# Performance work log

Hardware: AMD Instinct MI355X
Metric: run time of the kernel (lower is better)

Reference implementation:

```python
import jax, jax.numpy as jnp
import numpy as np

B, S, EMB, H = 4, 1024, 1024, 16
HD = EMB // H          # head_dim = 64
MAXP = 512             # RelativePositionalEncoder default max_position


def setup_inputs() -> dict:
    key = jax.random.key(0)
    ks = jax.random.split(key, 13)
    s = 1.0 / np.sqrt(EMB)  # xavier-ish scale keeps softmax logits sane
    return {
        "query": jax.random.normal(ks[0], (B, S, EMB), jnp.float32),
        "key": jax.random.normal(ks[1], (B, S, EMB), jnp.float32),
        "value": jax.random.normal(ks[2], (B, S, EMB), jnp.float32),
        "Wq": jax.random.normal(ks[3], (EMB, EMB), jnp.float32) * s,
        "bq": jnp.zeros((EMB,), jnp.float32),
        "Wk": jax.random.normal(ks[4], (EMB, EMB), jnp.float32) * s,
        "bk": jnp.zeros((EMB,), jnp.float32),
        "Wv": jax.random.normal(ks[5], (EMB, EMB), jnp.float32) * s,
        "bv": jnp.zeros((EMB,), jnp.float32),
        "Wo": jax.random.normal(ks[6], (EMB, EMB), jnp.float32) * s,
        "bo": jnp.zeros((EMB,), jnp.float32),
        "rel_k": jax.random.normal(ks[7], (2 * MAXP + 1, HD), jnp.float32) * 0.05,
        "rel_v": jax.random.normal(ks[8], (2 * MAXP + 1, HD), jnp.float32) * 0.05,
    }


def _split_heads(x):
    # [B,S,E] -> [B,S,H,HD] -> [B,H,S,HD] -> [B*H,S,HD]
    return x.reshape(B, S, H, HD).transpose(0, 2, 1, 3).reshape(B * H, S, HD)


def reference(query, key, value, Wq, bq, Wk, bk, Wv, bv, Wo, bo, rel_k, rel_v):
    scale = jnp.sqrt(jnp.asarray(HD, query.dtype))
    q = _split_heads(query @ Wq + bq)
    k = _split_heads(key @ Wk + bk)
    v = _split_heads(value @ Wv + bv)
    # relative position lookup tables: [Sq, Sk, HD]
    rp = jnp.clip(jnp.arange(S)[None, :] - jnp.arange(S)[:, None], -MAXP, MAXP) + MAXP
    a_key = rel_k[rp]
    a_value = rel_v[rp]
    qk = jnp.einsum('bqd,bkd->bqk', q, k)              # [B*H,S,S]
    rel_qk = jnp.einsum('bqd,qkd->bqk', q, a_key)      # relative score term
    attn = jax.nn.softmax((qk + rel_qk) / scale, axis=-1)
    out = jnp.einsum('bqk,bkd->bqd', attn, v) + jnp.einsum('bqk,qkd->bqd', attn, a_value)
    # faithful to original's view(num_heads, batch, -1, head_dim) then concat reshape
    out = out.reshape(H, B, S, HD).transpose(0, 2, 1, 3).reshape(B, S, H * HD)
    out = out @ Wo + bo
    return (out, attn)
```

## Files before the change

kernel.cpp:

```cpp
#include <hip/hip_runtime.h>


using s16x8 = __attribute__((ext_vector_type(8))) short;
using f32x4 = __attribute__((ext_vector_type(4))) float;

#define MFMA16 __builtin_amdgcn_mfma_f32_16x16x32_bf16

__device__ __forceinline__ float bf2f(unsigned short u) {
  union { unsigned int u; float f; } v; v.u = ((unsigned int)u) << 16; return v.f;
}
__device__ __forceinline__ unsigned short f2bf(float f) {
  union { float f; unsigned int u; } v; v.f = f;
  unsigned int r = (v.u + 0x7FFFu + ((v.u >> 16) & 1u)) >> 16;
  return (unsigned short)r;
}

__global__ void k_cvt_bf16(const float* __restrict__ in, unsigned short* __restrict__ out, int n) {
  int i = (blockIdx.x * 256 + threadIdx.x) * 8;
  if (i >= n) return;
  float4 a = *(const float4*)(in + i);
  float4 b = *(const float4*)(in + i + 4);
  s16x8 o;
  o[0] = (short)f2bf(a.x); o[1] = (short)f2bf(a.y); o[2] = (short)f2bf(a.z); o[3] = (short)f2bf(a.w);
  o[4] = (short)f2bf(b.x); o[5] = (short)f2bf(b.y); o[6] = (short)f2bf(b.z); o[7] = (short)f2bf(b.w);
  *(s16x8*)(out + i) = o;
}

__global__ void k_tr1024(const float* __restrict__ W, unsigned short* __restrict__ Wt) {
  __shared__ float t[32][33];
  int tx = threadIdx.x, ty = threadIdx.y;
  int n0 = blockIdx.x * 32, k0 = blockIdx.y * 32;
#pragma unroll
  for (int r = 0; r < 4; ++r)
    t[ty * 4 + r][tx] = W[(size_t)(k0 + ty * 4 + r) * 1024 + n0 + tx];
  __syncthreads();
#pragma unroll
  for (int r = 0; r < 4; ++r)
    Wt[(size_t)(n0 + ty * 4 + r) * 1024 + k0 + tx] = f2bf(t[tx][ty * 4 + r]);
}

__global__ void k_relprep(const float* __restrict__ rk, const float* __restrict__ rv,
                          unsigned short* __restrict__ relkb, unsigned short* __restrict__ rvTb) {
  int b = blockIdx.x;
  if (b < 33) {
    int i = (b * 256 + threadIdx.x) * 8;
    if (i < 65600) {
      float4 a = *(const float4*)(rk + i);
      float4 c = *(const float4*)(rk + i + 4);
      s16x8 o;
      o[0] = (short)f2bf(a.x); o[1] = (short)f2bf(a.y); o[2] = (short)f2bf(a.z); o[3] = (short)f2bf(a.w);
      o[4] = (short)f2bf(c.x); o[5] = (short)f2bf(c.y); o[6] = (short)f2bf(c.z); o[7] = (short)f2bf(c.w);
      *(s16x8*)(relkb + i) = o;
    }
  } else {
    int i = (b - 33) * 256 + threadIdx.x;
    if (i < 65600) {
      int p = i >> 6, d = i & 63;
      rvTb[d * 1040 + p] = f2bf(rv[i]);
    }
  }
}

__global__ __launch_bounds__(256)
void k_trV(const unsigned short* __restrict__ v, unsigned short* __restrict__ vt) {
  __shared__ unsigned short T[64][72];
  const int tid = threadIdx.x;
  const int bh = blockIdx.x >> 4;
  const int s0 = (blockIdx.x & 15) << 6;
  const int r = tid >> 2, cb = (tid & 3) << 4;
  const unsigned short* src = v + ((size_t)bh << 16) + (size_t)(s0 + r) * 64 + cb;
  *(s16x8*)&T[r][cb] = *(const s16x8*)src;
  *(s16x8*)&T[r][cb + 8] = *(const s16x8*)(src + 8);
  __syncthreads();
  unsigned short* dst = vt + ((size_t)bh << 16) + (size_t)r * 1024 + s0 + cb;
  s16x8 o0, o1;
#pragma unroll
  for (int e = 0; e < 8; ++e) o0[e] = T[cb + e][r];
#pragma unroll
  for (int e = 0; e < 8; ++e) o1[e] = T[cb + 8 + e][r];
  *(s16x8*)dst = o0;
  *(s16x8*)(dst + 8) = o1;
}

template <int MODE>
__global__ __launch_bounds__(256, 2)
void k_gemm(const unsigned short* __restrict__ A, const unsigned short* __restrict__ BT,
            const float* __restrict__ bias, void* __restrict__ Cout) {
  __shared__ alignas(16) unsigned short aT[2][4096];
  __shared__ alignas(16) unsigned short bT[2][2048];
  const int tid = threadIdx.x;
  const int lane = tid & 63;
  const int l15 = lane & 15, lhi = lane >> 4;
  const int w = tid >> 6;
  const int wr = w * 32;
  const int brow = blockIdx.y * 128, bcol = blockIdx.x * 64;
  f32x4 acc[2][4] = {};

#define STAGE(buf, kt) do {                                                              \
    int k0s = (kt) * 32;                                                                 \
    {                                                                                    \
      int c = tid;                                                                       \
      int row = c >> 2, k8 = (c & 3) * 8;                                                \
      __builtin_amdgcn_global_load_lds(                                                  \
        (const __attribute__((address_space(1))) void*)(A + (size_t)(brow + row) * 1024 + k0s + k8), \
        (__attribute__((address_space(3))) void*)(&aT[buf][c * 8]), 16, 0, 0);           \
      __builtin_amdgcn_global_load_lds(                                                  \
        (const __attribute__((address_space(1))) void*)(BT + (size_t)(bcol + row) * 1024 + k0s + k8),\
        (__attribute__((address_space(3))) void*)(&bT[buf][c * 8]), 16, 0, 0);           \
    }                                                                                    \
    {                                                                                    \
      int c = tid + 256;                                                                 \
      int row = c >> 2, k8 = (c & 3) * 8;                                                \
      __builtin_amdgcn_global_load_lds(                                                  \
        (const __attribute__((address_space(1))) void*)(A + (size_t)(brow + row) * 1024 + k0s + k8), \
        (__attribute__((address_space(3))) void*)(&aT[buf][c * 8]), 16, 0, 0);           \
    }                                                                                    \
  } while (0)

  int cur = 0;
  STAGE(0, 0);
  for (int kt = 0; kt < 32; ++kt) {
    __syncthreads();
    if (kt + 1 < 32) STAGE(cur ^ 1, kt + 1);
    s16x8 af[2], bfv[4];
#pragma unroll
    for (int m = 0; m < 2; ++m)
      af[m] = *(const s16x8*)&aT[cur][(wr + m * 16 + l15) * 32 + lhi * 8];
#pragma unroll
    for (int n = 0; n < 4; ++n)
      bfv[n] = *(const s16x8*)&bT[cur][(n * 16 + l15) * 32 + lhi * 8];
#pragma unroll
    for (int m = 0; m < 2; ++m)
#pragma unroll
      for (int n = 0; n < 4; ++n)
        acc[m][n] = MFMA16(af[m], bfv[n], acc[m][n], 0, 0, 0);
    __syncthreads();
    cur ^= 1;
  }
#undef STAGE

#pragma unroll
  for (int m = 0; m < 2; ++m) {
#pragma unroll
    for (int n = 0; n < 4; ++n) {
      int col = bcol + n * 16 + l15;
      float bs = bias[col];
#pragma unroll
      for (int j = 0; j < 4; ++j) {
        int r = brow + wr + m * 16 + lhi * 4 + j;
        float v = acc[m][n][j] + bs;
        if (MODE == 0) {
          int b = r >> 10, s = r & 1023, h = col >> 6, d = col & 63;
          ((unsigned short*)Cout)[(((size_t)((b << 4) + h) * 1024 + s) << 6) + d] = f2bf(v);
        } else {
          ((float*)Cout)[(size_t)r * 1024 + col] = v;
        }
      }
    }
  }
}

#define RPW 1032
#define PWP 520

__global__ __launch_bounds__(512, 3)
void k_attn(const unsigned short* __restrict__ qb, const unsigned short* __restrict__ kbm,
            const unsigned short* __restrict__ vT, const unsigned short* __restrict__ relk,
            const unsigned short* __restrict__ rvT, float* __restrict__ attn_out,
            unsigned short* __restrict__ xscr) {
  __shared__ alignas(16) unsigned short pbuf[16 * RPW];
  __shared__ alignas(16) unsigned short TbPw[16 * PWP];
  __shared__ float red[8][16];
  __shared__ float izS[16], plS[16], phS[16];
  __shared__ unsigned short bndS[32];

  const int tid = threadIdx.x;
  const int lane = tid & 63;
  const int w = tid >> 6;
  const int l15 = lane & 15, lhi = lane >> 4;
  const int orig = ((blockIdx.x & 7) << 9) | (blockIdx.x >> 3);
  const int bh = orig >> 6;
  const int q0 = (orig & 63) << 4;

  const unsigned short* Qh = qb + ((size_t)bh << 16);
  const unsigned short* Kh = kbm + ((size_t)bh << 16);
  const unsigned short* Vth = vT + ((size_t)bh << 16);

  const unsigned short* qp = Qh + (size_t)(q0 + l15) * 64 + lhi * 8;
  s16x8 qa0 = *(const s16x8*)qp;
  s16x8 qa1 = *(const s16x8*)(qp + 32);

  if (w == 0) {
    int sel = (l15 == 1) ? 1024 : 0;
    const unsigned short* rp = relk + (size_t)sel * 64 + lhi * 8;
    s16x8 rb0 = *(const s16x8*)rp;
    s16x8 rb1 = *(const s16x8*)(rp + 32);
    f32x4 d = {0.f, 0.f, 0.f, 0.f};
    d = MFMA16(qa0, rb0, d, 0, 0, 0);
    d = MFMA16(qa1, rb1, d, 0, 0, 0);
    if (l15 < 2) {
#pragma unroll
      for (int j = 0; j < 4; ++j) bndS[l15 * 16 + lhi * 4 + j] = f2bf(d[j]);
    }
  }

  float zp = 0.f;
  for (int half = 0; half < 2; ++half) {
    const int khalf = half << 9;
    __syncthreads();

    for (int i = tid; i < 16 * 64; i += 512) {
      int row = i >> 6, c8 = (i & 63) << 3;
      int fl = q0 + row - khalf - 512;
      unsigned short vlo = bndS[row], vhi = bndS[16 + row];
      s16x8 o;
#pragma unroll
      for (int e = 0; e < 8; ++e) o[e] = (short)((c8 + e < fl) ? vlo : vhi);
      *(s16x8*)&TbPw[row * PWP + c8] = o;
    }
    __syncthreads();

    {
      int pmin = khalf - q0 + 497;
      int PT0 = (pmin < 0 ? 0 : pmin) & ~15;
      int PT1 = khalf - q0 + 1023; if (PT1 > 1024) PT1 = 1024;
      for (int pt = PT0 + w * 16; pt <= PT1; pt += 128) {
        int pr = pt + l15; if (pr > 1024) pr = 1024;
        const unsigned short* rp = relk + (size_t)pr * 64 + lhi * 8;
        s16x8 rf0 = *(const s16x8*)rp;
        s16x8 rf1 = *(const s16x8*)(rp + 32);
        f32x4 d = {0.f, 0.f, 0.f, 0.f};
        d = MFMA16(qa0, rf0, d, 0, 0, 0);
        d = MFMA16(qa1, rf1, d, 0, 0, 0);
#pragma unroll
        for (int j = 0; j < 4; ++j) {
          int qi = lhi * 4 + j;
          int p = pt + l15;
          int u = p - khalf + q0 + qi - 512;
          if (p <= 1024 && u >= 0 && u < 512) TbPw[qi * PWP + u] = f2bf(d[j]);
        }
      }
    }
    __syncthreads();

    for (int n = 0; n < 4; ++n) {
      const int ktile = khalf + w * 16 + n * 128;
      const unsigned short* kp = Kh + (size_t)(ktile + l15) * 64 + lhi * 8;
      s16x8 kf0 = *(const s16x8*)kp;
      s16x8 kf1 = *(const s16x8*)(kp + 32);
      f32x4 c = {0.f, 0.f, 0.f, 0.f};
      __builtin_amdgcn_s_setprio(1);
      c = MFMA16(kf0, qa0, c, 0, 0, 0);
      c = MFMA16(kf1, qa1, c, 0, 0, 0);
      __builtin_amdgcn_s_setprio(0);
      uint2 tv = *(const uint2*)&TbPw[l15 * PWP + (ktile - khalf) + lhi * 4];
      float t0 = bf2f((unsigned short)(tv.x & 0xFFFF));
      float t1 = bf2f((unsigned short)(tv.x >> 16));
      float t2 = bf2f((unsigned short)(tv.y & 0xFFFF));
      float t3 = bf2f((unsigned short)(tv.y >> 16));
      float e0 = __expf((c[0] + t0) * 0.125f);
      float e1 = __expf((c[1] + t1) * 0.125f);
      float e2 = __expf((c[2] + t2) * 0.125f);
      float e3 = __expf((c[3] + t3) * 0.125f);
      zp += (e0 + e1) + (e2 + e3);
      uint2 pk;
      pk.x = (unsigned int)f2bf(e0) | ((unsigned int)f2bf(e1) << 16);
      pk.y = (unsigned int)f2bf(e2) | ((unsigned int)f2bf(e3) << 16);
      *(uint2*)&pbuf[l15 * RPW + ktile + lhi * 4] = pk;
    }
  }

  zp += __shfl_xor(zp, 16, 64);
  zp += __shfl_xor(zp, 32, 64);
  if (lane < 16) red[w][lane] = zp;
  __syncthreads();
  if (tid < 16) {
    float s = 0.f;
#pragma unroll
    for (int ww = 0; ww < 8; ++ww) s += red[ww][tid];
    izS[tid] = 1.0f / s;
  }

  {
    const int qi = tid >> 5, tq = tid & 31;
    const int qa = q0 + qi;
    int lo, hi;
    const bool isPh = (qa < 512);
    if (isPh) { lo = qa + 512; hi = 1024; }
    else      { lo = 0;        hi = qa - 511; }
    float s = 0.f;
    const unsigned short* srow = pbuf + qi * RPW;
    const int kb0 = lo & ~7;
    for (int k8 = kb0 + tq * 8; k8 < hi; k8 += 256) {
      s16x8 v8 = *(const s16x8*)&srow[k8];
#pragma unroll
      for (int e = 0; e < 8; ++e) {
        int k = k8 + e;
        s += (k >= lo && k < hi) ? bf2f((unsigned short)v8[e]) : 0.f;
      }
    }
#pragma unroll
    for (int off = 1; off < 32; off <<= 1) s += __shfl_xor(s, off, 64);
    if (tq == 0) { plS[qi] = isPh ? 0.f : s; phS[qi] = isPh ? s : 0.f; }
  }
  __syncthreads();

  {
    float* ao = attn_out + ((size_t)bh << 20) + ((size_t)q0 << 10);
#pragma unroll
    for (int n = 0; n < 4; ++n) {
      int idx = n * 512 + tid;
      int row = idx >> 7, c8 = (idx & 127) << 3;
      float iz = izS[row];
      s16x8 p8 = *(const s16x8*)&pbuf[row * RPW + c8];
      f32x4 o0, o1;
      o0[0] = bf2f((unsigned short)p8[0]) * iz; o0[1] = bf2f((unsigned short)p8[1]) * iz;
      o0[2] = bf2f((unsigned short)p8[2]) * iz; o0[3] = bf2f((unsigned short)p8[3]) * iz;
      o1[0] = bf2f((unsigned short)p8[4]) * iz; o1[1] = bf2f((unsigned short)p8[5]) * iz;
      o1[2] = bf2f((unsigned short)p8[6]) * iz; o1[3] = bf2f((unsigned short)p8[7]) * iz;
      __builtin_nontemporal_store(o0, (f32x4*)(ao + (row << 10) + c8));
      __builtin_nontemporal_store(o1, (f32x4*)(ao + (row << 10) + c8 + 4));
    }
  }

  f32x4 acc = {0.f, 0.f, 0.f, 0.f};
  const int d0 = (w >> 1) << 4;
  const int kbase = (w & 1) << 9;
  const unsigned short* vrow = Vth + (size_t)(d0 + l15) * 1024 + lhi * 8;
#pragma unroll 8
  for (int kc = kbase; kc < kbase + 512; kc += 32) {
    s16x8 pa = *(const s16x8*)&pbuf[l15 * RPW + kc + lhi * 8];
    s16x8 vf = *(const s16x8*)(vrow + kc);
    acc = MFMA16(pa, vf, acc, 0, 0, 0);
  }

  const unsigned short* rrow = rvT + (size_t)(d0 + l15) * 1040 + lhi * 8;
  {
    const int sqi = tid >> 5, stq = tid & 31;
    const int ssh = sqi & 7, shs = ssh >> 1;
    const bool sodd = (ssh & 1) != 0;
    unsigned short* drow = TbPw + sqi * PWP;
    const unsigned short* srow = pbuf + sqi * RPW;
    const int kq = (w & 1) << 8;
    for (int ph = 0; ph < 2; ++ph) {
      __syncthreads();
      const int base = q0 + sqi + (ph ? 0 : -512);
      for (int t = stq; t < 64; t += 32) {
        const int kw0 = base + t * 8;
        s16x8 o;
        if (kw0 >= 0 && kw0 + 8 <= 1024) {
          const int A = kw0 - ssh;
          union { s16x8 v; unsigned int u[4]; } a0, a1, ov;
          a0.v = *(const s16x8*)&srow[A];
          a1.v = *(const s16x8*)&srow[A + 8];
          unsigned int wd[8];
#pragma unroll
          for (int j2 = 0; j2 < 4; ++j2) { wd[j2] = a0.u[j2]; wd[4 + j2] = a1.u[j2]; }
          unsigned int v7[7];
#pragma unroll
          for (int j2 = 0; j2 < 7; ++j2) {
            unsigned int sf = (wd[j2] >> 16) | (wd[j2 + 1] << 16);
            v7[j2] = sodd ? sf : wd[j2];
          }
#pragma unroll
          for (int j2 = 0; j2 < 4; ++j2) {
            unsigned int t0 = (shs & 1) ? v7[j2 + 1] : v7[j2];
            unsigned int t1 = (shs & 1) ? v7[j2 + 3] : v7[j2 + 2];
            ov.u[j2] = (shs & 2) ? t1 : t0;
          }
          o = ov.v;
        } else if (kw0 + 8 <= 0 || kw0 >= 1024) {
          o = (s16x8){0, 0, 0, 0, 0, 0, 0, 0};
        } else {
#pragma unroll
          for (int e = 0; e < 8; ++e) {
            int k = kw0 + e;
            int kc2 = k < 0 ? 0 : (k > 1023 ? 1023 : k);
            unsigned short vv = srow[kc2];
            o[e] = (k >= 0 && k < 1024) ? (short)vv : (short)0;
          }
        }
        *(s16x8*)&drow[t * 8] = o;
        if (ph == 0 && t == 0) drow[0] = f2bf(plS[sqi]);
      }
      __syncthreads();
#pragma unroll 8
      for (int kc = kq; kc < kq + 256; kc += 32) {
        s16x8 pa = *(const s16x8*)&TbPw[l15 * PWP + kc + lhi * 8];
        s16x8 rb = *(const s16x8*)(rrow + (ph << 9) + kc);
        acc = MFMA16(pa, rb, acc, 0, 0, 0);
      }
    }
  }

  __syncthreads();
  float* fscr = (float*)TbPw;
  if (w & 1) {
    f32x4* dst = (f32x4*)&fscr[(((w >> 1) << 6) | lane) << 2];
    *dst = acc;
  }
  __syncthreads();
  if (!(w & 1)) {
    f32x4 other = *(const f32x4*)&fscr[(((w >> 1) << 6) | lane) << 2];
    float rv1024 = bf2f(rvT[(size_t)(d0 + l15) * 1040 + 1024]);
    const size_t fb = ((size_t)(bh >> 2) << 18) + ((size_t)(bh & 3) << 6);
#pragma unroll
    for (int j = 0; j < 4; ++j) {
      int qi = lhi * 4 + j;
      float v = (acc[j] + other[j] + phS[qi] * rv1024) * izS[qi];
      xscr[fb + ((size_t)(q0 + qi) << 8) + d0 + l15] = f2bf(v);
    }
  }
}

extern "C" void kernel_launch(void* const* d_in, const int* in_sizes, int n_in,
                              void* d_out, int out_size, void* d_ws, size_t ws_size,
                              hipStream_t stream) {
  (void)in_sizes; (void)n_in; (void)out_size; (void)ws_size;
  const float* query = (const float*)d_in[0];
  const float* key   = (const float*)d_in[1];
  const float* value = (const float*)d_in[2];
  const float* Wq = (const float*)d_in[3];
  const float* bq = (const float*)d_in[4];
  const float* Wk = (const float*)d_in[5];
  const float* bk = (const float*)d_in[6];
  const float* Wv = (const float*)d_in[7];
  const float* bv = (const float*)d_in[8];
  const float* Wo = (const float*)d_in[9];
  const float* bo = (const float*)d_in[10];
  const float* rel_k = (const float*)d_in[11];
  const float* rel_v = (const float*)d_in[12];

  char* ws = (char*)d_ws;
  const size_t MB = 1024 * 1024;
  unsigned short* qb    = (unsigned short*)(ws);
  unsigned short* kbuf  = (unsigned short*)(ws + 8 * MB);
  unsigned short* vbuf  = (unsigned short*)(ws + 16 * MB);
  unsigned short* tmp16 = (unsigned short*)(ws + 24 * MB);
  unsigned short* wt    = (unsigned short*)(ws + 32 * MB);
  unsigned short* relkb = (unsigned short*)(ws + 34 * MB);
  unsigned short* rvTb  = (unsigned short*)(ws + 34 * MB + 512 * 1024);
  unsigned short* vTb   = tmp16;
  unsigned short* xscr  = vbuf;

  float* out0 = (float*)d_out;
  float* attn_out = out0 + 4194304;

  dim3 trb(32, 8), trg(32, 32);
  dim3 gg(16, 32);

  k_relprep<<<290, 256, 0, stream>>>(rel_k, rel_v, relkb, rvTb);

  k_cvt_bf16<<<2048, 256, 0, stream>>>(query, tmp16, 4194304);
  k_tr1024<<<trg, trb, 0, stream>>>(Wq, wt);
  k_gemm<0><<<gg, 256, 0, stream>>>(tmp16, wt, bq, qb);

  k_cvt_bf16<<<2048, 256, 0, stream>>>(key, tmp16, 4194304);
  k_tr1024<<<trg, trb, 0, stream>>>(Wk, wt);
  k_gemm<0><<<gg, 256, 0, stream>>>(tmp16, wt, bk, kbuf);

  k_cvt_bf16<<<2048, 256, 0, stream>>>(value, tmp16, 4194304);
  k_tr1024<<<trg, trb, 0, stream>>>(Wv, wt);
  k_gemm<0><<<gg, 256, 0, stream>>>(tmp16, wt, bv, vbuf);

  k_trV<<<1024, 256, 0, stream>>>(vbuf, vTb);
  k_tr1024<<<trg, trb, 0, stream>>>(Wo, wt);

  k_attn<<<4096, 512, 0, stream>>>(qb, kbuf, vTb, relkb, rvTb, attn_out, xscr);

  k_gemm<1><<<gg, 256, 0, stream>>>(xscr, wt, bo, out0);
}
```

Measured before the change: 380.6 us.

## Fuse weight prep, batch QKV GEMMs with in-loop fp32 conversion, trim attention setup

Merges the four weight transposes and the rel-table prep into one launch. The three Q/K/V GEMMs become a single 3D-grid launch that reads fp32 activations directly and converts them to bf16 in registers, which removes the separate conversion kernels and the bf16 round-trip through memory. In the attention kernel, the boundary-fill precompute of the rel-key band is dropped in favour of index clamping, K fragments are prefetched one tile ahead, and the occupancy hint is raised from 3 to 5 blocks. The trade-offs are extra register pressure from the fused conversion and prefetch, and a larger weight workspace.

```diff
diff --git a/kernel.cpp b/kernel.cpp
--- a/kernel.cpp
+++ b/kernel.cpp
@@ -15,48 +15,47 @@
   return (unsigned short)r;
 }
 
-__global__ void k_cvt_bf16(const float* __restrict__ in, unsigned short* __restrict__ out, int n) {
-  int i = (blockIdx.x * 256 + threadIdx.x) * 8;
-  if (i >= n) return;
-  float4 a = *(const float4*)(in + i);
-  float4 b = *(const float4*)(in + i + 4);
-  s16x8 o;
-  o[0] = (short)f2bf(a.x); o[1] = (short)f2bf(a.y); o[2] = (short)f2bf(a.z); o[3] = (short)f2bf(a.w);
-  o[4] = (short)f2bf(b.x); o[5] = (short)f2bf(b.y); o[6] = (short)f2bf(b.z); o[7] = (short)f2bf(b.w);
-  *(s16x8*)(out + i) = o;
-}
-
-__global__ void k_tr1024(const float* __restrict__ W, unsigned short* __restrict__ Wt) {
-  __shared__ float t[32][33];
-  int tx = threadIdx.x, ty = threadIdx.y;
-  int n0 = blockIdx.x * 32, k0 = blockIdx.y * 32;
-#pragma unroll
-  for (int r = 0; r < 4; ++r)
-    t[ty * 4 + r][tx] = W[(size_t)(k0 + ty * 4 + r) * 1024 + n0 + tx];
-  __syncthreads();
-#pragma unroll
-  for (int r = 0; r < 4; ++r)
-    Wt[(size_t)(n0 + ty * 4 + r) * 1024 + k0 + tx] = f2bf(t[tx][ty * 4 + r]);
-}
-
-__global__ void k_relprep(const float* __restrict__ rk, const float* __restrict__ rv,
-                          unsigned short* __restrict__ relkb, unsigned short* __restrict__ rvTb) {
-  int b = blockIdx.x;
-  if (b < 33) {
-    int i = (b * 256 + threadIdx.x) * 8;
-    if (i < 65600) {
-      float4 a = *(const float4*)(rk + i);
-      float4 c = *(const float4*)(rk + i + 4);
-      s16x8 o;
-      o[0] = (short)f2bf(a.x); o[1] = (short)f2bf(a.y); o[2] = (short)f2bf(a.z); o[3] = (short)f2bf(a.w);
-      o[4] = (short)f2bf(c.x); o[5] = (short)f2bf(c.y); o[6] = (short)f2bf(c.z); o[7] = (short)f2bf(c.w);
-      *(s16x8*)(relkb + i) = o;
-    }
+__global__ __launch_bounds__(256)
+void k_prep(const float* __restrict__ Wq, const float* __restrict__ Wk,
+            const float* __restrict__ Wv, const float* __restrict__ Wo,
+            unsigned short* __restrict__ wqt, unsigned short* __restrict__ wkt,
+            unsigned short* __restrict__ wvt, unsigned short* __restrict__ wot,
+            const float* __restrict__ rk, const float* __restrict__ rv,
+            unsigned short* __restrict__ relkb, unsigned short* __restrict__ rvTb) {
+  const int b = blockIdx.x;
+  const int tid = threadIdx.x;
+  if (b < 4096) {
+    __shared__ float t[32][33];
+    const int sel = b >> 10, idx = b & 1023;
+    const float* W = sel == 0 ? Wq : (sel == 1 ? Wk : (sel == 2 ? Wv : Wo));
+    unsigned short* Wt = sel == 0 ? wqt : (sel == 1 ? wkt : (sel == 2 ? wvt : wot));
+    const int n0 = (idx & 31) * 32, k0 = (idx >> 5) * 32;
+    const int tx = tid & 31, ty = tid >> 5;
+#pragma unroll
+    for (int r = 0; r < 4; ++r)
+      t[ty * 4 + r][tx] = W[(size_t)(k0 + ty * 4 + r) * 1024 + n0 + tx];
+    __syncthreads();
+#pragma unroll
+    for (int r = 0; r < 4; ++r)
+      Wt[(size_t)(n0 + ty * 4 + r) * 1024 + k0 + tx] = f2bf(t[tx][ty * 4 + r]);
   } else {
-    int i = (b - 33) * 256 + threadIdx.x;
-    if (i < 65600) {
-      int p = i >> 6, d = i & 63;
-      rvTb[d * 1040 + p] = f2bf(rv[i]);
+    const int b2 = b - 4096;
+    if (b2 < 33) {
+      int i = (b2 * 256 + tid) * 8;
+      if (i < 65600) {
+        float4 a = *(const float4*)(rk + i);
+        float4 c = *(const float4*)(rk + i + 4);
+        s16x8 o;
+        o[0] = (short)f2bf(a.x); o[1] = (short)f2bf(a.y); o[2] = (short)f2bf(a.z); o[3] = (short)f2bf(a.w);
+        o[4] = (short)f2bf(c.x); o[5] = (short)f2bf(c.y); o[6] = (short)f2bf(c.z); o[7] = (short)f2bf(c.w);
+        *(s16x8*)(relkb + i) = o;
+      }
+    } else {
+      int i = (b2 - 33) * 256 + tid;
+      if (i < 65600) {
+        int p = i >> 6, d = i & 63;
+        rvTb[d * 1040 + p] = f2bf(rv[i]);
+      }
     }
   }
 }
@@ -82,10 +81,108 @@
   *(s16x8*)(dst + 8) = o1;
 }
 
-template <int MODE>
 __global__ __launch_bounds__(256, 2)
-void k_gemm(const unsigned short* __restrict__ A, const unsigned short* __restrict__ BT,
-            const float* __restrict__ bias, void* __restrict__ Cout) {
+void k_gemm_qkv(const float* __restrict__ Aq, const float* __restrict__ Ak, const float* __restrict__ Av,
+                const unsigned short* __restrict__ Wq_, const unsigned short* __restrict__ Wk_,
+                const unsigned short* __restrict__ Wv_,
+                const float* __restrict__ bq_, const float* __restrict__ bk_, const float* __restrict__ bv_,
+                unsigned short* __restrict__ Oq, unsigned short* __restrict__ Ok,
+                unsigned short* __restrict__ Ov) {
+  const int z = blockIdx.z;
+  const float* A = z == 0 ? Aq : (z == 1 ? Ak : Av);
+  const unsigned short* BT = z == 0 ? Wq_ : (z == 1 ? Wk_ : Wv_);
+  const float* bias = z == 0 ? bq_ : (z == 1 ? bk_ : bv_);
+  unsigned short* Cout = z == 0 ? Oq : (z == 1 ? Ok : Ov);
+
+  __shared__ alignas(16) unsigned short aT[2][4096];
+  __shared__ alignas(16) unsigned short bT[2][2048];
+  const int tid = threadIdx.x;
+  const int lane = tid & 63;
+  const int l15 = lane & 15, lhi = lane >> 4;
+  const int w = tid >> 6;
+  const int wr = w * 32;
+  const int brow = blockIdx.y * 128, bcol = blockIdx.x * 64;
+  f32x4 acc[2][4] = {};
+
+  const int c1 = tid, c2 = tid + 256;
+  const int r1 = c1 >> 2, kA1 = (c1 & 3) * 8;
+  const int r2 = c2 >> 2, kA2 = (c2 & 3) * 8;
+  float4 a0, a1, a2, a3;
+  s16x8 w1v, w2v;
+
+#define LOADA(kt) do {                                                     \
+    const float* p1 = A + (size_t)(brow + r1) * 1024 + (kt) * 32 + kA1;    \
+    a0 = *(const float4*)p1; a1 = *(const float4*)(p1 + 4);                \
+    const float* p2 = A + (size_t)(brow + r2) * 1024 + (kt) * 32 + kA2;    \
+    a2 = *(const float4*)p2; a3 = *(const float4*)(p2 + 4);                \
+  } while (0)
+#define CVTA() do {                                                        \
+    w1v[0] = (short)f2bf(a0.x); w1v[1] = (short)f2bf(a0.y);                \
+    w1v[2] = (short)f2bf(a0.z); w1v[3] = (short)f2bf(a0.w);                \
+    w1v[4] = (short)f2bf(a1.x); w1v[5] = (short)f2bf(a1.y);                \
+    w1v[6] = (short)f2bf(a1.z); w1v[7] = (short)f2bf(a1.w);                \
+    w2v[0] = (short)f2bf(a2.x); w2v[1] = (short)f2bf(a2.y);                \
+    w2v[2] = (short)f2bf(a2.z); w2v[3] = (short)f2bf(a2.w);                \
+    w2v[4] = (short)f2bf(a3.x); w2v[5] = (short)f2bf(a3.y);                \
+    w2v[6] = (short)f2bf(a3.z); w2v[7] = (short)f2bf(a3.w);                \
+  } while (0)
+#define WRA(buf) do {                                                      \
+    *(s16x8*)&aT[buf][c1 * 8] = w1v;                                       \
+    *(s16x8*)&aT[buf][c2 * 8] = w2v;                                       \
+  } while (0)
+#define GLB(buf, kt) do {                                                  \
+    int row = c1 >> 2, k8 = (c1 & 3) * 8;                                  \
+    __builtin_amdgcn_global_load_lds(                                      \
+      (const __attribute__((address_space(1))) void*)(BT + (size_t)(bcol + row) * 1024 + (kt) * 32 + k8), \
+      (__attribute__((address_space(3))) void*)(&bT[buf][c1 * 8]), 16, 0, 0); \
+  } while (0)
+
+  LOADA(0); GLB(0, 0); CVTA(); WRA(0);
+  int cur = 0;
+  for (int kt = 0; kt < 32; ++kt) {
+    __syncthreads();
+    if (kt + 1 < 32) { LOADA(kt + 1); GLB(cur ^ 1, kt + 1); }
+    s16x8 af[2], bfv[4];
+#pragma unroll
+    for (int m = 0; m < 2; ++m)
+      af[m] = *(const s16x8*)&aT[cur][(wr + m * 16 + l15) * 32 + lhi * 8];
+#pragma unroll
+    for (int n = 0; n < 4; ++n)
+      bfv[n] = *(const s16x8*)&bT[cur][(n * 16 + l15) * 32 + lhi * 8];
+#pragma unroll
+    for (int m = 0; m < 2; ++m)
+#pragma unroll
+      for (int n = 0; n < 4; ++n)
+        acc[m][n] = MFMA16(af[m], bfv[n], acc[m][n], 0, 0, 0);
+    if (kt + 1 < 32) { CVTA(); WRA(cur ^ 1); }
+    __syncthreads();
+    cur ^= 1;
+  }
+#undef LOADA
+#undef CVTA
+#undef WRA
+#undef GLB
+
+#pragma unroll
+  for (int m = 0; m < 2; ++m) {
+#pragma unroll
+    for (int n = 0; n < 4; ++n) {
+      int col = bcol + n * 16 + l15;
+      float bs = bias[col];
+#pragma unroll
+      for (int j = 0; j < 4; ++j) {
+        int r = brow + wr + m * 16 + lhi * 4 + j;
+        float v = acc[m][n][j] + bs;
+        int bb = r >> 10, s = r & 1023, h = col >> 6, d = col & 63;
+        Cout[(((size_t)((bb << 4) + h) * 1024 + s) << 6) + d] = f2bf(v);
+      }
+    }
+  }
+}
+
+__global__ __launch_bounds__(256, 2)
+void k_gemm_o(const unsigned short* __restrict__ A, const unsigned short* __restrict__ BT,
+              const float* __restrict__ bias, float* __restrict__ Cout) {
   __shared__ alignas(16) unsigned short aT[2][4096];
   __shared__ alignas(16) unsigned short bT[2][2048];
   const int tid = threadIdx.x;
@@ -148,13 +245,7 @@
 #pragma unroll
       for (int j = 0; j < 4; ++j) {
         int r = brow + wr + m * 16 + lhi * 4 + j;
-        float v = acc[m][n][j] + bs;
-        if (MODE == 0) {
-          int b = r >> 10, s = r & 1023, h = col >> 6, d = col & 63;
-          ((unsigned short*)Cout)[(((size_t)((b << 4) + h) * 1024 + s) << 6) + d] = f2bf(v);
-        } else {
-          ((float*)Cout)[(size_t)r * 1024 + col] = v;
-        }
+        Cout[(size_t)r * 1024 + col] = acc[m][n][j] + bs;
       }
     }
   }
@@ -163,7 +254,7 @@
 #define RPW 1032
 #define PWP 520
 
-__global__ __launch_bounds__(512, 3)
+__global__ __launch_bounds__(512, 5)
 void k_attn(const unsigned short* __restrict__ qb, const unsigned short* __restrict__ kbm,
             const unsigned short* __restrict__ vT, const unsigned short* __restrict__ relk,
             const unsigned short* __restrict__ rvT, float* __restrict__ attn_out,
@@ -172,7 +263,6 @@
   __shared__ alignas(16) unsigned short TbPw[16 * PWP];
   __shared__ float red[8][16];
   __shared__ float izS[16], plS[16], phS[16];
-  __shared__ unsigned short bndS[32];
 
   const int tid = threadIdx.x;
   const int lane = tid & 63;
@@ -190,42 +280,16 @@
   s16x8 qa0 = *(const s16x8*)qp;
   s16x8 qa1 = *(const s16x8*)(qp + 32);
 
-  if (w == 0) {
-    int sel = (l15 == 1) ? 1024 : 0;
-    const unsigned short* rp = relk + (size_t)sel * 64 + lhi * 8;
-    s16x8 rb0 = *(const s16x8*)rp;
-    s16x8 rb1 = *(const s16x8*)(rp + 32);
-    f32x4 d = {0.f, 0.f, 0.f, 0.f};
-    d = MFMA16(qa0, rb0, d, 0, 0, 0);
-    d = MFMA16(qa1, rb1, d, 0, 0, 0);
-    if (l15 < 2) {
-#pragma unroll
-      for (int j = 0; j < 4; ++j) bndS[l15 * 16 + lhi * 4 + j] = f2bf(d[j]);
-    }
-  }
-
   float zp = 0.f;
   for (int half = 0; half < 2; ++half) {
     const int khalf = half << 9;
     __syncthreads();
 
-    for (int i = tid; i < 16 * 64; i += 512) {
-      int row = i >> 6, c8 = (i & 63) << 3;
-      int fl = q0 + row - khalf - 512;
-      unsigned short vlo = bndS[row], vhi = bndS[16 + row];
-      s16x8 o;
-#pragma unroll
-      for (int e = 0; e < 8; ++e) o[e] = (short)((c8 + e < fl) ? vlo : vhi);
-      *(s16x8*)&TbPw[row * PWP + c8] = o;
-    }
-    __syncthreads();
-
     {
-      int pmin = khalf - q0 + 497;
-      int PT0 = (pmin < 0 ? 0 : pmin) & ~15;
-      int PT1 = khalf - q0 + 1023; if (PT1 > 1024) PT1 = 1024;
+      const int PT0 = ((khalf - q0 + 497) >> 4) << 4;
+      const int PT1 = khalf - q0 + 1023;
       for (int pt = PT0 + w * 16; pt <= PT1; pt += 128) {
-        int pr = pt + l15; if (pr > 1024) pr = 1024;
+        int pr = pt + l15; pr = pr < 0 ? 0 : (pr > 1024 ? 1024 : pr);
         const unsigned short* rp = relk + (size_t)pr * 64 + lhi * 8;
         s16x8 rf0 = *(const s16x8*)rp;
         s16x8 rf1 = *(const s16x8*)(rp + 32);
@@ -235,24 +299,33 @@
 #pragma unroll
         for (int j = 0; j < 4; ++j) {
           int qi = lhi * 4 + j;
-          int p = pt + l15;
-          int u = p - khalf + q0 + qi - 512;
-          if (p <= 1024 && u >= 0 && u < 512) TbPw[qi * PWP + u] = f2bf(d[j]);
+          int u = pt + l15 - khalf + q0 + qi - 512;
+          if (u >= 0 && u < 512) TbPw[qi * PWP + u] = f2bf(d[j]);
         }
       }
     }
     __syncthreads();
 
+    const unsigned short* kbp = Kh + (size_t)(khalf + w * 16 + l15) * 64 + lhi * 8;
+    s16x8 ka0 = *(const s16x8*)kbp;
+    s16x8 ka1 = *(const s16x8*)(kbp + 32);
+    s16x8 kb0 = *(const s16x8*)(kbp + 128 * 64);
+    s16x8 kb1 = *(const s16x8*)(kbp + 128 * 64 + 32);
+#pragma unroll
     for (int n = 0; n < 4; ++n) {
       const int ktile = khalf + w * 16 + n * 128;
-      const unsigned short* kp = Kh + (size_t)(ktile + l15) * 64 + lhi * 8;
-      s16x8 kf0 = *(const s16x8*)kp;
-      s16x8 kf1 = *(const s16x8*)(kp + 32);
+      s16x8 kf0 = (n & 1) ? kb0 : ka0;
+      s16x8 kf1 = (n & 1) ? kb1 : ka1;
       f32x4 c = {0.f, 0.f, 0.f, 0.f};
       __builtin_amdgcn_s_setprio(1);
       c = MFMA16(kf0, qa0, c, 0, 0, 0);
       c = MFMA16(kf1, qa1, c, 0, 0, 0);
       __builtin_amdgcn_s_setprio(0);
+      if (n < 2) {
+        const unsigned short* np = kbp + (n + 2) * 128 * 64;
+        if (n & 1) { kb0 = *(const s16x8*)np; kb1 = *(const s16x8*)(np + 32); }
+        else       { ka0 = *(const s16x8*)np; ka1 = *(const s16x8*)(np + 32); }
+      }
       uint2 tv = *(const uint2*)&TbPw[l15 * PWP + (ktile - khalf) + lhi * 4];
       float t0 = bf2f((unsigned short)(tv.x & 0xFFFF));
       float t1 = bf2f((unsigned short)(tv.x >> 16));
@@ -290,8 +363,8 @@
     else      { lo = 0;        hi = qa - 511; }
     float s = 0.f;
     const unsigned short* srow = pbuf + qi * RPW;
-    const int kb0 = lo & ~7;
-    for (int k8 = kb0 + tq * 8; k8 < hi; k8 += 256) {
+    const int kb0i = lo & ~7;
+    for (int k8 = kb0i + tq * 8; k8 < hi; k8 += 256) {
       s16x8 v8 = *(const s16x8*)&srow[k8];
 #pragma unroll
       for (int e = 0; e < 8; ++e) {
@@ -350,12 +423,12 @@
         s16x8 o;
         if (kw0 >= 0 && kw0 + 8 <= 1024) {
           const int A = kw0 - ssh;
-          union { s16x8 v; unsigned int u[4]; } a0, a1, ov;
-          a0.v = *(const s16x8*)&srow[A];
-          a1.v = *(const s16x8*)&srow[A + 8];
+          union { s16x8 v; unsigned int u[4]; } a0u, a1u, ov;
+          a0u.v = *(const s16x8*)&srow[A];
+          a1u.v = *(const s16x8*)&srow[A + 8];
           unsigned int wd[8];
 #pragma unroll
-          for (int j2 = 0; j2 < 4; ++j2) { wd[j2] = a0.u[j2]; wd[4 + j2] = a1.u[j2]; }
+          for (int j2 = 0; j2 < 4; ++j2) { wd[j2] = a0u.u[j2]; wd[4 + j2] = a1u.u[j2]; }
           unsigned int v7[7];
 #pragma unroll
           for (int j2 = 0; j2 < 7; ++j2) {
@@ -436,37 +509,29 @@
   unsigned short* qb    = (unsigned short*)(ws);
   unsigned short* kbuf  = (unsigned short*)(ws + 8 * MB);
   unsigned short* vbuf  = (unsigned short*)(ws + 16 * MB);
-  unsigned short* tmp16 = (unsigned short*)(ws + 24 * MB);
-  unsigned short* wt    = (unsigned short*)(ws + 32 * MB);
-  unsigned short* relkb = (unsigned short*)(ws + 34 * MB);
-  unsigned short* rvTb  = (unsigned short*)(ws + 34 * MB + 512 * 1024);
-  unsigned short* vTb   = tmp16;
+  unsigned short* vTb   = (unsigned short*)(ws + 24 * MB);
+  unsigned short* wqt   = (unsigned short*)(ws + 32 * MB);
+  unsigned short* wkt   = (unsigned short*)(ws + 34 * MB);
+  unsigned short* wvt   = (unsigned short*)(ws + 36 * MB);
+  unsigned short* wot   = (unsigned short*)(ws + 38 * MB);
+  unsigned short* relkb = (unsigned short*)(ws + 40 * MB);
+  unsigned short* rvTb  = (unsigned short*)(ws + 40 * MB + 256 * 1024);
   unsigned short* xscr  = vbuf;
 
   float* out0 = (float*)d_out;
   float* attn_out = out0 + 4194304;
 
-  dim3 trb(32, 8), trg(32, 32);
-  dim3 gg(16, 32);
-
-  k_relprep<<<290, 256, 0, stream>>>(rel_k, rel_v, relkb, rvTb);
-
-  k_cvt_bf16<<<2048, 256, 0, stream>>>(query, tmp16, 4194304);
-  k_tr1024<<<trg, trb, 0, stream>>>(Wq, wt);
-  k_gemm<0><<<gg, 256, 0, stream>>>(tmp16, wt, bq, qb);
-
-  k_cvt_bf16<<<2048, 256, 0, stream>>>(key, tmp16, 4194304);
-  k_tr1024<<<trg, trb, 0, stream>>>(Wk, wt);
-  k_gemm<0><<<gg, 256, 0, stream>>>(tmp16, wt, bk, kbuf);
-
-  k_cvt_bf16<<<2048, 256, 0, stream>>>(value, tmp16, 4194304);
-  k_tr1024<<<trg, trb, 0, stream>>>(Wv, wt);
-  k_gemm<0><<<gg, 256, 0, stream>>>(tmp16, wt, bv, vbuf);
+  k_prep<<<4386, 256, 0, stream>>>(Wq, Wk, Wv, Wo, wqt, wkt, wvt, wot,
+                                   rel_k, rel_v, relkb, rvTb);
+
+  k_gemm_qkv<<<dim3(16, 32, 3), 256, 0, stream>>>(query, key, value,
+                                                  wqt, wkt, wvt,
+                                                  bq, bk, bv,
+                                                  qb, kbuf, vbuf);
 
   k_trV<<<1024, 256, 0, stream>>>(vbuf, vTb);
-  k_tr1024<<<trg, trb, 0, stream>>>(Wo, wt);
 
   k_attn<<<4096, 512, 0, stream>>>(qb, kbuf, vTb, relkb, rvTb, attn_out, xscr);
 
-  k_gemm<1><<<gg, 256, 0, stream>>>(xscr, wt, bo, out0);
-}
+  k_gemm_o<<<dim3(16, 32), 256, 0, stream>>>(xscr, wot, bo, out0);
+}
```

Measured after the change: 365.4 us. 4.0% less time.
